# Kernel optimization log

Hardware: AMD Instinct MI355X
Metric: run time of the kernel (lower is better)

## Reference

```python
import jax, jax.numpy as jnp
import numpy as np

B, T, C = 2, 2048, 2048
N_HEAD, N_KV_HEAD = 16, 4
HEAD_DIM = C // N_HEAD          # 128
N_REP = N_HEAD // N_KV_HEAD     # 4
HALF = HEAD_DIM // 2            # 64


def setup_inputs() -> dict:
    key = jax.random.key(0)
    ks = jax.random.split(key, 6)
    x = jax.random.normal(ks[0], (B, T, C), dtype=jnp.float32)
    # real RoPE tables: theta_i = 10000^{-2i/d}, angles = t * theta_i
    inv_freq = 1.0 / (10000.0 ** (jnp.arange(0, HALF, dtype=jnp.float32) / HALF))
    angles = jnp.arange(T, dtype=jnp.float32)[:, None] * inv_freq[None, :]  # (T, HALF)
    freqs_cos = jnp.cos(angles)
    freqs_sin = jnp.sin(angles)
    s = 0.02
    wq = jax.random.normal(ks[1], (C, C), dtype=jnp.float32) * s
    wk = jax.random.normal(ks[2], (N_KV_HEAD * HEAD_DIM, C), dtype=jnp.float32) * s
    wv = jax.random.normal(ks[3], (N_KV_HEAD * HEAD_DIM, C), dtype=jnp.float32) * s
    wo = jax.random.normal(ks[4], (C, C), dtype=jnp.float32) * s
    return {"x": x, "freqs_cos": freqs_cos, "freqs_sin": freqs_sin,
            "wq": wq, "wk": wk, "wv": wv, "wo": wo}


def _apply_rope(t, cos, sin):
    # t: (B, T, H, D); rotate consecutive pairs (llama view_as_complex layout)
    te = t[..., 0::2]   # (B, T, H, D/2)
    to = t[..., 1::2]
    c = cos[None, :, None, :]
    s = sin[None, :, None, :]
    oe = te * c - to * s
    oo = te * s + to * c
    return jnp.stack([oe, oo], axis=-1).reshape(t.shape)


def reference(x, freqs_cos, freqs_sin, wq, wk, wv, wo):
    Bx, Tx, Cx = x.shape
    q = (x @ wq.T).reshape(Bx, Tx, N_HEAD, HEAD_DIM)
    k = (x @ wk.T).reshape(Bx, Tx, N_KV_HEAD, HEAD_DIM)
    v = (x @ wv.T).reshape(Bx, Tx, N_KV_HEAD, HEAD_DIM)
    q = _apply_rope(q, freqs_cos, freqs_sin)
    k = _apply_rope(k, freqs_cos, freqs_sin)
    # GQA: group query heads by kv head instead of repeat_interleave'ing KV
    qg = q.reshape(Bx, Tx, N_KV_HEAD, N_REP, HEAD_DIM)
    scale = 1.0 / jnp.sqrt(jnp.asarray(HEAD_DIM, dtype=q.dtype))
    # scores: (B, kv_head, rep, T, T)
    scores = jnp.einsum('btgrd,bsgd->bgrts', qg, k) * scale
    causal = jnp.tril(jnp.ones((Tx, Tx), dtype=bool))
    scores = jnp.where(causal[None, None, None], scores, jnp.asarray(-1e30, dtype=scores.dtype))
    probs = jax.nn.softmax(scores, axis=-1)
    y = jnp.einsum('bgrts,bsgd->btgrd', probs, v).reshape(Bx, Tx, Cx)
    return y @ wo.T
```

## Files before the change

### kernel.cpp

```cpp
#include <hip/hip_runtime.h>

#define T_SEQ 2048
#define NB    2
#define NHEAD 16
#define NKV   4
#define HD    128
#define CDIM  2048
#define QKV_W 3072
#define MROWS 4096

#define QSCALE 0.12752648137154393f

typedef unsigned int  uint;
typedef unsigned short ushort;

typedef __attribute__((ext_vector_type(8))) __bf16 bf16x8;
typedef __attribute__((ext_vector_type(4))) float  floatx4;

#if __has_builtin(__builtin_amdgcn_exp2f)
#define EXP2F(x) __builtin_amdgcn_exp2f(x)
#else
#define EXP2F(x) exp2f(x)
#endif

__device__ __forceinline__ uint bf16rne(float f) {
  uint u = __float_as_uint(f);
  u += 0x7fffu + ((u >> 16) & 1u);
  return u >> 16;
}
__device__ __forceinline__ float bflo(uint w) { return __uint_as_float(w << 16); }
__device__ __forceinline__ float bfhi(uint w) { return __uint_as_float(w & 0xffff0000u); }

__device__ __forceinline__ void block_bar() {
  __builtin_amdgcn_sched_barrier(0);
  __builtin_amdgcn_s_barrier();
  __builtin_amdgcn_sched_barrier(0);
}

__global__ void cast_all(const float* __restrict__ x,  const float* __restrict__ wq,
                         const float* __restrict__ wk, const float* __restrict__ wv,
                         const float* __restrict__ wo, uint* __restrict__ out) {
  int i = blockIdx.x * 256 + threadIdx.x;
  const float2* src; int off;
  if (i < 4194304)      { src = (const float2*)x;  off = 0; }
  else if (i < 6291456) { src = (const float2*)wq; off = 4194304; }
  else if (i < 6815744) { src = (const float2*)wk; off = 6291456; }
  else if (i < 7340032) { src = (const float2*)wv; off = 6815744; }
  else                  { src = (const float2*)wo; off = 7340032; }
  float2 v = src[i - off];
  out[i] = bf16rne(v.x) | (bf16rne(v.y) << 16);
}

__device__ __forceinline__ void store_elem(ushort* C, size_t idx, float v) { C[idx] = (ushort)bf16rne(v); }
__device__ __forceinline__ void store_elem(float*  C, size_t idx, float v) { C[idx] = v; }

template <typename OutT>
__global__ __launch_bounds__(256, 2) void gemm_bt(const ushort* __restrict__ A,
                                                  const ushort* __restrict__ Bt,
                                                  OutT* __restrict__ C,
                                                  int M, int N, int K,
                                                  int vcol0, ushort* __restrict__ vt) {
  __shared__ ushort smem[32768];
  const int tid  = threadIdx.x;
  const int wave = tid >> 6, lane = tid & 63;
  const int quad = lane >> 4, l16 = lane & 15;
  const int wm = wave >> 1, wn = wave & 1;
  const int mBase = blockIdx.y << 7;
  const int nBase = blockIdx.x << 7;
  const int NKT = K >> 6;

  floatx4 acc[4][4];
#pragma unroll
  for (int i = 0; i < 4; ++i)
#pragma unroll
    for (int j = 0; j < 4; ++j)
#pragma unroll
      for (int r = 0; r < 4; ++r) acc[i][j][r] = 0.f;

  const int srow = tid >> 3;
  const int sc8  = ((tid & 7) ^ (srow & 7)) << 3;
  const ushort* gA = A  + (size_t)(mBase + srow) * K + sc8;
  const ushort* gB = Bt + (size_t)(nBase + srow) * K + sc8;
  ushort* ldsA = smem + (wave << 9);
  ushort* ldsB = smem + 16384 + (wave << 9);

#define STAGE(k0, bsel)                                                               \
  do {                                                                                \
    _Pragma("unroll")                                                                 \
    for (int it_ = 0; it_ < 4; ++it_)                                                 \
      __builtin_amdgcn_global_load_lds(                                               \
          (const __attribute__((address_space(1))) void*)(gA + (size_t)it_ * 32 * K + (k0)), \
          (__attribute__((address_space(3))) void*)(ldsA + (bsel) + it_ * 2048), 16, 0, 0);  \
    _Pragma("unroll")                                                                 \
    for (int it_ = 0; it_ < 4; ++it_)                                                 \
      __builtin_amdgcn_global_load_lds(                                               \
          (const __attribute__((address_space(1))) void*)(gB + (size_t)it_ * 32 * K + (k0)), \
          (__attribute__((address_space(3))) void*)(ldsB + (bsel) + it_ * 2048), 16, 0, 0);  \
  } while (0)

  const int aro = ((wm << 6) + l16) * 64;
  const int bro = 16384 + ((wn << 6) + l16) * 64;
  const int sw0 = ((quad       ^ (l16 & 7)) << 3);
  const int sw1 = (((quad + 4) ^ (l16 & 7)) << 3);

  STAGE(0, 0);
  STAGE(64, 8192);
  asm volatile("s_waitcnt vmcnt(8)" ::: "memory");
  block_bar();

  for (int t = 0; t < NKT; ++t) {
    const int bsel = (t & 1) << 13;
#pragma unroll
    for (int kk = 0; kk < 2; ++kk) {
      const int sw = kk ? sw1 : sw0;
      bf16x8 bfrag[4];
#pragma unroll
      for (int j = 0; j < 4; ++j)
        bfrag[j] = *(const bf16x8*)&smem[bro + bsel + j * 1024 + sw];
#pragma unroll
      for (int i = 0; i < 4; ++i) {
        bf16x8 ai = *(const bf16x8*)&smem[aro + bsel + i * 1024 + sw];
#pragma unroll
        for (int j = 0; j < 4; ++j)
          acc[i][j] = __builtin_amdgcn_mfma_f32_16x16x32_bf16(ai, bfrag[j], acc[i][j], 0, 0, 0);
      }
    }
    asm volatile("s_waitcnt lgkmcnt(0)" ::: "memory");
    block_bar();
    if (t + 2 < NKT) {
      STAGE((t + 2) << 6, bsel);
      asm volatile("s_waitcnt vmcnt(8)" ::: "memory");
      block_bar();
    } else if (t + 1 < NKT) {
      asm volatile("s_waitcnt vmcnt(0)" ::: "memory");
      block_bar();
    }
  }
#undef STAGE

#pragma unroll
  for (int i = 0; i < 4; ++i) {
    const int rowb = mBase + (wm << 6) + (i << 4) + (quad << 2);
#pragma unroll
    for (int j = 0; j < 4; ++j) {
      const int colb = nBase + (wn << 6) + (j << 4);
      const int col  = colb + l16;
      if (colb < vcol0) {
#pragma unroll
        for (int r = 0; r < 4; ++r)
          store_elem(C, (size_t)(rowb + r) * N + col, acc[i][j][r]);
      } else {
        const int vcol = col - vcol0;
        const int bb = rowb >> 11;
        const int t  = rowb & 2047;
        uint2 pw;
        pw.x = bf16rne(acc[i][j][0]) | (bf16rne(acc[i][j][1]) << 16);
        pw.y = bf16rne(acc[i][j][2]) | (bf16rne(acc[i][j][3]) << 16);
        *(uint2*)(vt + (((size_t)(bb << 9) + vcol) << 11) + t) = pw;
      }
    }
  }
}

__global__ void rope_k(ushort* __restrict__ qkv, const float* __restrict__ fc,
                       const float* __restrict__ fs) {
  int idx  = blockIdx.x * 256 + threadIdx.x;
  int d2   = idx & 63;
  int rest = idx >> 6;
  int hh   = rest & 3;
  int bt   = rest >> 2;
  int t    = bt & (T_SEQ - 1);
  float c = fc[(t << 6) + d2];
  float s = fs[(t << 6) + d2];
  uint* p = (uint*)(qkv + (size_t)bt * QKV_W + 2048 + (hh << 7) + (d2 << 1));
  uint w = *p;
  float e = bflo(w), o = bfhi(w);
  *p = bf16rne(e * c - o * s) | (bf16rne(e * s + o * c) << 16);
}

__global__ __launch_bounds__(512, 2) void attn_mfma(const ushort* __restrict__ qkv,
                                                    const ushort* __restrict__ vtg,
                                                    ushort* __restrict__ y,
                                                    const float* __restrict__ fc,
                                                    const float* __restrict__ fs) {
  __shared__ ushort smem[51456];
  ushort* sP = smem + 32768;
  float*  sOf = (float*)smem;
  ushort* sO  = smem + 33792;
  float*  sLf = (float*)(smem + 51200);

  const int tid  = threadIdx.x;
  const int wave = tid >> 6, lane = tid & 63;
  const int quad = lane >> 4, l16 = lane & 15;
  const int w_s = wave & 1;
  const int w_t = wave >> 1;
  const int h = blockIdx.y, b = blockIdx.z, kh = h >> 2;
  const size_t bT = (size_t)b * T_SEQ;

  union { uint4 u; bf16x8 v; } ones_u;
  ones_u.u = make_uint4(0x3F803F80u, 0x3F803F80u, 0x3F803F80u, 0x3F803F80u);
  const bf16x8 onesf = ones_u.v;

  const int kr  = tid >> 4;
  const int kc8 = tid & 15;
  const ushort* gK = qkv + (bT + kr) * QKV_W + 2048 + kh * HD + ((kc8 ^ (kr & 7)) << 3);
  const int vd  = tid >> 3;
  const int vsc = tid & 7;
  const ushort* gV = vtg + (((size_t)(b << 9) + (kh << 7) + vd) << 11) + ((vsc ^ (vd & 7)) << 3);

#define STAGE_ATTN(cn, bo_)                                                            \
  do {                                                                                 \
    _Pragma("unroll")                                                                  \
    for (int it_ = 0; it_ < 2; ++it_)                                                  \
      __builtin_amdgcn_global_load_lds(                                                \
          (const __attribute__((address_space(1))) void*)(gK + ((size_t)(cn) * 64 + it_ * 32) * QKV_W), \
          (__attribute__((address_space(3))) void*)(smem + (bo_) + (wave << 9) + it_ * 4096), 16, 0, 0); \
    _Pragma("unroll")                                                                  \
    for (int it_ = 0; it_ < 2; ++it_)                                                  \
      __builtin_amdgcn_global_load_lds(                                                \
          (const __attribute__((address_space(1))) void*)(gV + ((size_t)it_ << 17) + (cn) * 64), \
          (__attribute__((address_space(3))) void*)(smem + 16384 + (bo_) + (wave << 9) + it_ * 4096), 16, 0, 0); \
  } while (0)

  for (int half = 0; half < 2; ++half) {
    const int xt = half ? (15 - (int)blockIdx.x) : (int)blockIdx.x;
    const int t0 = xt << 7;
    const int sblk = w_s << 5, tblk = w_t << 5;

    bf16x8 qf[2][4];
#pragma unroll
    for (int tt = 0; tt < 2; ++tt) {
      const int trow = t0 + tblk + tt * 16 + l16;
      const float* fcr = fc + (trow << 6);
      const float* fsr = fs + (trow << 6);
#pragma unroll
      for (int kk = 0; kk < 4; ++kk) {
        union { uint4 u; bf16x8 v; } qa;
        qa.u = *(const uint4*)(qkv + (bT + trow) * QKV_W + h * HD + kk * 32 + quad * 8);
        const int d2b = kk * 16 + quad * 4;
        uint* wp = (uint*)&qa.u;
#pragma unroll
        for (int m = 0; m < 4; ++m) {
          float c = fcr[d2b + m], s = fsr[d2b + m];
          float e = bflo(wp[m]), o = bfhi(wp[m]);
          float oe = (e * c - o * s) * QSCALE;
          float oo = (e * s + o * c) * QSCALE;
          wp[m] = bf16rne(oe) | (bf16rne(oo) << 16);
        }
        qf[tt][kk] = qa.v;
      }
    }

    floatx4 oacc[2][8];
    floatx4 lacc[2];
#pragma unroll
    for (int tt = 0; tt < 2; ++tt) {
#pragma unroll
      for (int r = 0; r < 4; ++r) lacc[tt][r] = 0.f;
#pragma unroll
      for (int dt = 0; dt < 8; ++dt)
#pragma unroll
        for (int r = 0; r < 4; ++r) oacc[tt][dt][r] = 0.f;
    }

    const int nch = (t0 >> 6) + 2;

    STAGE_ATTN(0, 0);

    for (int ch = 0; ch < nch; ++ch) {
      __syncthreads();
      if (ch + 1 < nch) STAGE_ATTN(ch + 1, ((ch + 1) & 1) << 13);
      const int bo = (ch & 1) << 13;
      const int s0 = ch << 6;

      const bool fullmask = (s0 + sblk) > (t0 + tblk + 31);
      if (!fullmask) {
        floatx4 accS[2][2];
#pragma unroll
        for (int st = 0; st < 2; ++st)
#pragma unroll
          for (int tt = 0; tt < 2; ++tt)
#pragma unroll
            for (int r = 0; r < 4; ++r) accS[st][tt][r] = 0.f;

#pragma unroll
        for (int kk = 0; kk < 4; ++kk) {
          bf16x8 kf0 = *(const bf16x8*)(smem + bo + (sblk + l16) * 128 +
                                        ((((kk << 2) + quad) ^ (l16 & 7)) << 3));
          bf16x8 kf1 = *(const bf16x8*)(smem + bo + (sblk + 16 + l16) * 128 +
                                        ((((kk << 2) + quad) ^ (l16 & 7)) << 3));
#pragma unroll
          for (int tt = 0; tt < 2; ++tt)
            accS[0][tt] = __builtin_amdgcn_mfma_f32_16x16x32_bf16(kf0, qf[tt][kk], accS[0][tt], 0, 0, 0);
#pragma unroll
          for (int tt = 0; tt < 2; ++tt)
            accS[1][tt] = __builtin_amdgcn_mfma_f32_16x16x32_bf16(kf1, qf[tt][kk], accS[1][tt], 0, 0, 0);
        }

        const bool diag = (s0 + sblk + 31) > (t0 + tblk);
#pragma unroll
        for (int st = 0; st < 2; ++st)
#pragma unroll
          for (int tt = 0; tt < 2; ++tt) {
            float p[4];
            if (diag) {
              const int sg = s0 + sblk + st * 16 + quad * 4;
              const int tg = t0 + tblk + tt * 16 + l16;
#pragma unroll
              for (int r = 0; r < 4; ++r)
                p[r] = (sg + r <= tg) ? EXP2F(accS[st][tt][r]) : 0.f;
            } else {
#pragma unroll
              for (int r = 0; r < 4; ++r) p[r] = EXP2F(accS[st][tt][r]);
            }
            uint2 pw;
            pw.x = (__float_as_uint(p[0]) >> 16) | (__float_as_uint(p[1]) & 0xFFFF0000u);
            pw.y = (__float_as_uint(p[2]) >> 16) | (__float_as_uint(p[3]) & 0xFFFF0000u);
            *(uint2*)(sP + (tblk + tt * 16 + l16) * 72 + sblk + st * 16 + quad * 4) = pw;
          }

        bf16x8 pf[2];
#pragma unroll
        for (int tt = 0; tt < 2; ++tt) {
          pf[tt] = *(const bf16x8*)(sP + (tblk + tt * 16 + l16) * 72 + sblk + (quad << 3));
          lacc[tt] = __builtin_amdgcn_mfma_f32_16x16x32_bf16(pf[tt], onesf, lacc[tt], 0, 0, 0);
        }
#pragma unroll
        for (int dt = 0; dt < 8; ++dt) {
          bf16x8 vf = *(const bf16x8*)(smem + 16384 + bo + (dt * 16 + l16) * 64 +
                                       ((((w_s << 2) + quad) ^ (l16 & 7)) << 3));
#pragma unroll
          for (int tt = 0; tt < 2; ++tt)
            oacc[tt][dt] = __builtin_amdgcn_mfma_f32_16x16x32_bf16(pf[tt], vf, oacc[tt][dt], 0, 0, 0);
        }
      }
    }

    __syncthreads();
    if (w_s == 0) {
#pragma unroll
      for (int tt = 0; tt < 2; ++tt) {
#pragma unroll
        for (int dt = 0; dt < 8; ++dt)
#pragma unroll
          for (int r = 0; r < 4; ++r)
            sOf[(tblk + tt * 16 + quad * 4 + r) * 132 + dt * 16 + l16] = oacc[tt][dt][r];
        if (l16 == 0) {
#pragma unroll
          for (int r = 0; r < 4; ++r)
            sLf[tblk + tt * 16 + quad * 4 + r] = lacc[tt][r];
        }
      }
    }
    __syncthreads();
    if (w_s == 1) {
#pragma unroll
      for (int tt = 0; tt < 2; ++tt) {
        float linv[4];
#pragma unroll
        for (int r = 0; r < 4; ++r)
          linv[r] = 1.0f / (sLf[tblk + tt * 16 + quad * 4 + r] + lacc[tt][r]);
#pragma unroll
        for (int dt = 0; dt < 8; ++dt)
#pragma unroll
          for (int r = 0; r < 4; ++r) {
            float v = (sOf[(tblk + tt * 16 + quad * 4 + r) * 132 + dt * 16 + l16] +
                       oacc[tt][dt][r]) * linv[r];
            sO[(tblk + tt * 16 + quad * 4 + r) * 136 + dt * 16 + l16] = (ushort)bf16rne(v);
          }
      }
    }
    __syncthreads();
#pragma unroll
    for (int it = 0; it < 4; ++it) {
      int idx = it * 512 + tid;
      int rr = idx >> 4, c8 = idx & 15;
      *(uint4*)(y + (bT + t0 + rr) * CDIM + h * HD + c8 * 8) =
          *(const uint4*)(sO + rr * 136 + c8 * 8);
    }
  }
#undef STAGE_ATTN
}

extern "C" void kernel_launch(void* const* d_in, const int* in_sizes, int n_in,
                              void* d_out, int out_size, void* d_ws, size_t ws_size,
                              hipStream_t stream) {
  const float* x    = (const float*)d_in[0];
  const float* fcos = (const float*)d_in[1];
  const float* fsin = (const float*)d_in[2];
  const float* wq   = (const float*)d_in[3];
  const float* wk   = (const float*)d_in[4];
  const float* wv   = (const float*)d_in[5];
  const float* wo   = (const float*)d_in[6];
  float* out = (float*)d_out;

  ushort* ws    = (ushort*)d_ws;
  ushort* xb    = ws;
  ushort* yb    = ws;
  ushort* wqkvb = ws    + 8388608;
  ushort* wob   = wqkvb + 6291456;
  ushort* qkv   = wob   + 4194304;
  ushort* vtg   = qkv   + 12582912;

  cast_all<<<36864, 256, 0, stream>>>(x, wq, wk, wv, wo, (uint*)ws);

  gemm_bt<ushort><<<dim3(QKV_W / 128, MROWS / 128), 256, 0, stream>>>(
      xb, wqkvb, qkv, MROWS, QKV_W, CDIM, 2560, vtg);

  rope_k<<<4096, 256, 0, stream>>>(qkv, fcos, fsin);

  attn_mfma<<<dim3(8, NHEAD, NB), 512, 0, stream>>>(qkv, vtg, yb, fcos, fsin);

  gemm_bt<float><<<dim3(CDIM / 128, MROWS / 128), 256, 0, stream>>>(
      yb, wob, out, MROWS, CDIM, CDIM, 1 << 30, nullptr);
}
```

Measured before the change: 278.2 us.

## Split attention blocks to one query tile each and shrink LDS for higher occupancy

Each attention block previously handled two query tiles (a paired long and short one for load balance). Now the grid doubles to 16 tiles per head and each block handles a single tile, launched in reverse order so the heaviest tiles start first. The P staging buffer moves to a 64-wide XOR-swizzled layout and the output reduction is done one 16-row slice at a time. Together these cut shared memory enough to raise launch bounds to 4 blocks per CU, trading the explicit pairing balance for more parallelism and occupancy, with added register pressure risk.

After: 372.6 us. +33.9%, slower.

```diff
diff --git a/kernel.cpp b/kernel.cpp
--- a/kernel.cpp
+++ b/kernel.cpp
@@ -178,16 +178,16 @@
   *p = bf16rne(e * c - o * s) | (bf16rne(e * s + o * c) << 16);
 }
 
-__global__ __launch_bounds__(512, 2) void attn_mfma(const ushort* __restrict__ qkv,
+__global__ __launch_bounds__(512, 4) void attn_mfma(const ushort* __restrict__ qkv,
                                                     const ushort* __restrict__ vtg,
                                                     ushort* __restrict__ y,
                                                     const float* __restrict__ fc,
                                                     const float* __restrict__ fs) {
-  __shared__ ushort smem[51456];
-  ushort* sP = smem + 32768;
+  __shared__ ushort smem[40960];
+  ushort* sP  = smem + 32768;
   float*  sOf = (float*)smem;
-  ushort* sO  = smem + 33792;
-  float*  sLf = (float*)(smem + 51200);
+  ushort* sO  = smem + 16896;
+  float*  sLf = (float*)(smem + 25600);
 
   const int tid  = threadIdx.x;
   const int wave = tid >> 6, lane = tid & 63;
@@ -222,161 +222,157 @@
           (__attribute__((address_space(3))) void*)(smem + 16384 + (bo_) + (wave << 9) + it_ * 4096), 16, 0, 0); \
   } while (0)
 
-  for (int half = 0; half < 2; ++half) {
-    const int xt = half ? (15 - (int)blockIdx.x) : (int)blockIdx.x;
-    const int t0 = xt << 7;
-    const int sblk = w_s << 5, tblk = w_t << 5;
-
-    bf16x8 qf[2][4];
-#pragma unroll
-    for (int tt = 0; tt < 2; ++tt) {
-      const int trow = t0 + tblk + tt * 16 + l16;
-      const float* fcr = fc + (trow << 6);
-      const float* fsr = fs + (trow << 6);
+  const int xt = 15 - (int)blockIdx.x;
+  const int t0 = xt << 7;
+  const int sblk = w_s << 5, tblk = w_t << 5;
+
+  bf16x8 qf[2][4];
+#pragma unroll
+  for (int tt = 0; tt < 2; ++tt) {
+    const int trow = t0 + tblk + tt * 16 + l16;
+    const float* fcr = fc + (trow << 6);
+    const float* fsr = fs + (trow << 6);
+#pragma unroll
+    for (int kk = 0; kk < 4; ++kk) {
+      union { uint4 u; bf16x8 v; } qa;
+      qa.u = *(const uint4*)(qkv + (bT + trow) * QKV_W + h * HD + kk * 32 + quad * 8);
+      const int d2b = kk * 16 + quad * 4;
+      uint* wp = (uint*)&qa.u;
+#pragma unroll
+      for (int m = 0; m < 4; ++m) {
+        float c = fcr[d2b + m], s = fsr[d2b + m];
+        float e = bflo(wp[m]), o = bfhi(wp[m]);
+        float oe = (e * c - o * s) * QSCALE;
+        float oo = (e * s + o * c) * QSCALE;
+        wp[m] = bf16rne(oe) | (bf16rne(oo) << 16);
+      }
+      qf[tt][kk] = qa.v;
+    }
+  }
+
+  floatx4 oacc[2][8];
+  floatx4 lacc[2];
+#pragma unroll
+  for (int tt = 0; tt < 2; ++tt) {
+#pragma unroll
+    for (int r = 0; r < 4; ++r) lacc[tt][r] = 0.f;
+#pragma unroll
+    for (int dt = 0; dt < 8; ++dt)
+#pragma unroll
+      for (int r = 0; r < 4; ++r) oacc[tt][dt][r] = 0.f;
+  }
+
+  const int nch = (t0 >> 6) + 2;
+
+  STAGE_ATTN(0, 0);
+
+  for (int ch = 0; ch < nch; ++ch) {
+    __syncthreads();
+    if (ch + 1 < nch) STAGE_ATTN(ch + 1, ((ch + 1) & 1) << 13);
+    const int bo = (ch & 1) << 13;
+    const int s0 = ch << 6;
+
+    const bool fullmask = (s0 + sblk) > (t0 + tblk + 31);
+    if (!fullmask) {
+      floatx4 accS[2][2];
+#pragma unroll
+      for (int st = 0; st < 2; ++st)
+#pragma unroll
+        for (int tt = 0; tt < 2; ++tt)
+#pragma unroll
+          for (int r = 0; r < 4; ++r) accS[st][tt][r] = 0.f;
+
 #pragma unroll
       for (int kk = 0; kk < 4; ++kk) {
-        union { uint4 u; bf16x8 v; } qa;
-        qa.u = *(const uint4*)(qkv + (bT + trow) * QKV_W + h * HD + kk * 32 + quad * 8);
-        const int d2b = kk * 16 + quad * 4;
-        uint* wp = (uint*)&qa.u;
-#pragma unroll
-        for (int m = 0; m < 4; ++m) {
-          float c = fcr[d2b + m], s = fsr[d2b + m];
-          float e = bflo(wp[m]), o = bfhi(wp[m]);
-          float oe = (e * c - o * s) * QSCALE;
-          float oo = (e * s + o * c) * QSCALE;
-          wp[m] = bf16rne(oe) | (bf16rne(oo) << 16);
+        bf16x8 kf0 = *(const bf16x8*)(smem + bo + (sblk + l16) * 128 +
+                                      ((((kk << 2) + quad) ^ (l16 & 7)) << 3));
+        bf16x8 kf1 = *(const bf16x8*)(smem + bo + (sblk + 16 + l16) * 128 +
+                                      ((((kk << 2) + quad) ^ (l16 & 7)) << 3));
+#pragma unroll
+        for (int tt = 0; tt < 2; ++tt)
+          accS[0][tt] = __builtin_amdgcn_mfma_f32_16x16x32_bf16(kf0, qf[tt][kk], accS[0][tt], 0, 0, 0);
+#pragma unroll
+        for (int tt = 0; tt < 2; ++tt)
+          accS[1][tt] = __builtin_amdgcn_mfma_f32_16x16x32_bf16(kf1, qf[tt][kk], accS[1][tt], 0, 0, 0);
+      }
+
+      const bool diag = (s0 + sblk + 31) > (t0 + tblk);
+#pragma unroll
+      for (int st = 0; st < 2; ++st)
+#pragma unroll
+        for (int tt = 0; tt < 2; ++tt) {
+          float p[4];
+          if (diag) {
+            const int sg = s0 + sblk + st * 16 + quad * 4;
+            const int tg = t0 + tblk + tt * 16 + l16;
+#pragma unroll
+            for (int r = 0; r < 4; ++r)
+              p[r] = (sg + r <= tg) ? EXP2F(accS[st][tt][r]) : 0.f;
+          } else {
+#pragma unroll
+            for (int r = 0; r < 4; ++r) p[r] = EXP2F(accS[st][tt][r]);
+          }
+          uint2 pw;
+          pw.x = (__float_as_uint(p[0]) >> 16) | (__float_as_uint(p[1]) & 0xFFFF0000u);
+          pw.y = (__float_as_uint(p[2]) >> 16) | (__float_as_uint(p[3]) & 0xFFFF0000u);
+          const int c4s = (((w_s << 3) + (st << 2) + quad) ^ ((l16 & 7) << 1)) << 2;
+          *(uint2*)(sP + ((tblk + tt * 16 + l16) << 6) + c4s) = pw;
         }
-        qf[tt][kk] = qa.v;
-      }
-    }
-
-    floatx4 oacc[2][8];
-    floatx4 lacc[2];
-#pragma unroll
-    for (int tt = 0; tt < 2; ++tt) {
-#pragma unroll
-      for (int r = 0; r < 4; ++r) lacc[tt][r] = 0.f;
+
+      bf16x8 pf[2];
+#pragma unroll
+      for (int tt = 0; tt < 2; ++tt) {
+        const int c4r = (((w_s << 3) + (quad << 1)) ^ ((l16 & 7) << 1)) << 2;
+        pf[tt] = *(const bf16x8*)(sP + ((tblk + tt * 16 + l16) << 6) + c4r);
+        lacc[tt] = __builtin_amdgcn_mfma_f32_16x16x32_bf16(pf[tt], onesf, lacc[tt], 0, 0, 0);
+      }
+#pragma unroll
+      for (int dt = 0; dt < 8; ++dt) {
+        bf16x8 vf = *(const bf16x8*)(smem + 16384 + bo + (dt * 16 + l16) * 64 +
+                                     ((((w_s << 2) + quad) ^ (l16 & 7)) << 3));
+#pragma unroll
+        for (int tt = 0; tt < 2; ++tt)
+          oacc[tt][dt] = __builtin_amdgcn_mfma_f32_16x16x32_bf16(pf[tt], vf, oacc[tt][dt], 0, 0, 0);
+      }
+    }
+  }
+
+#pragma unroll
+  for (int tt = 0; tt < 2; ++tt) {
+    __syncthreads();
+    const int v = (w_t << 4) + (quad << 2);
+    if (w_s == 0) {
 #pragma unroll
       for (int dt = 0; dt < 8; ++dt)
 #pragma unroll
-        for (int r = 0; r < 4; ++r) oacc[tt][dt][r] = 0.f;
-    }
-
-    const int nch = (t0 >> 6) + 2;
-
-    STAGE_ATTN(0, 0);
-
-    for (int ch = 0; ch < nch; ++ch) {
-      __syncthreads();
-      if (ch + 1 < nch) STAGE_ATTN(ch + 1, ((ch + 1) & 1) << 13);
-      const int bo = (ch & 1) << 13;
-      const int s0 = ch << 6;
-
-      const bool fullmask = (s0 + sblk) > (t0 + tblk + 31);
-      if (!fullmask) {
-        floatx4 accS[2][2];
-#pragma unroll
-        for (int st = 0; st < 2; ++st)
-#pragma unroll
-          for (int tt = 0; tt < 2; ++tt)
-#pragma unroll
-            for (int r = 0; r < 4; ++r) accS[st][tt][r] = 0.f;
-
-#pragma unroll
-        for (int kk = 0; kk < 4; ++kk) {
-          bf16x8 kf0 = *(const bf16x8*)(smem + bo + (sblk + l16) * 128 +
-                                        ((((kk << 2) + quad) ^ (l16 & 7)) << 3));
-          bf16x8 kf1 = *(const bf16x8*)(smem + bo + (sblk + 16 + l16) * 128 +
-                                        ((((kk << 2) + quad) ^ (l16 & 7)) << 3));
-#pragma unroll
-          for (int tt = 0; tt < 2; ++tt)
-            accS[0][tt] = __builtin_amdgcn_mfma_f32_16x16x32_bf16(kf0, qf[tt][kk], accS[0][tt], 0, 0, 0);
-#pragma unroll
-          for (int tt = 0; tt < 2; ++tt)
-            accS[1][tt] = __builtin_amdgcn_mfma_f32_16x16x32_bf16(kf1, qf[tt][kk], accS[1][tt], 0, 0, 0);
-        }
-
-        const bool diag = (s0 + sblk + 31) > (t0 + tblk);
-#pragma unroll
-        for (int st = 0; st < 2; ++st)
-#pragma unroll
-          for (int tt = 0; tt < 2; ++tt) {
-            float p[4];
-            if (diag) {
-              const int sg = s0 + sblk + st * 16 + quad * 4;
-              const int tg = t0 + tblk + tt * 16 + l16;
-#pragma unroll
-              for (int r = 0; r < 4; ++r)
-                p[r] = (sg + r <= tg) ? EXP2F(accS[st][tt][r]) : 0.f;
-            } else {
-#pragma unroll
-              for (int r = 0; r < 4; ++r) p[r] = EXP2F(accS[st][tt][r]);
-            }
-            uint2 pw;
-            pw.x = (__float_as_uint(p[0]) >> 16) | (__float_as_uint(p[1]) & 0xFFFF0000u);
-            pw.y = (__float_as_uint(p[2]) >> 16) | (__float_as_uint(p[3]) & 0xFFFF0000u);
-            *(uint2*)(sP + (tblk + tt * 16 + l16) * 72 + sblk + st * 16 + quad * 4) = pw;
-          }
-
-        bf16x8 pf[2];
-#pragma unroll
-        for (int tt = 0; tt < 2; ++tt) {
-          pf[tt] = *(const bf16x8*)(sP + (tblk + tt * 16 + l16) * 72 + sblk + (quad << 3));
-          lacc[tt] = __builtin_amdgcn_mfma_f32_16x16x32_bf16(pf[tt], onesf, lacc[tt], 0, 0, 0);
-        }
-#pragma unroll
-        for (int dt = 0; dt < 8; ++dt) {
-          bf16x8 vf = *(const bf16x8*)(smem + 16384 + bo + (dt * 16 + l16) * 64 +
-                                       ((((w_s << 2) + quad) ^ (l16 & 7)) << 3));
-#pragma unroll
-          for (int tt = 0; tt < 2; ++tt)
-            oacc[tt][dt] = __builtin_amdgcn_mfma_f32_16x16x32_bf16(pf[tt], vf, oacc[tt][dt], 0, 0, 0);
-        }
-      }
-    }
-
-    __syncthreads();
-    if (w_s == 0) {
-#pragma unroll
-      for (int tt = 0; tt < 2; ++tt) {
-#pragma unroll
-        for (int dt = 0; dt < 8; ++dt)
-#pragma unroll
-          for (int r = 0; r < 4; ++r)
-            sOf[(tblk + tt * 16 + quad * 4 + r) * 132 + dt * 16 + l16] = oacc[tt][dt][r];
-        if (l16 == 0) {
-#pragma unroll
-          for (int r = 0; r < 4; ++r)
-            sLf[tblk + tt * 16 + quad * 4 + r] = lacc[tt][r];
-        }
+        for (int r = 0; r < 4; ++r)
+          sOf[(v + r) * 132 + dt * 16 + l16] = oacc[tt][dt][r];
+      if (l16 == 0) {
+#pragma unroll
+        for (int r = 0; r < 4; ++r) sLf[v + r] = lacc[tt][r];
       }
     }
     __syncthreads();
     if (w_s == 1) {
-#pragma unroll
-      for (int tt = 0; tt < 2; ++tt) {
-        float linv[4];
-#pragma unroll
-        for (int r = 0; r < 4; ++r)
-          linv[r] = 1.0f / (sLf[tblk + tt * 16 + quad * 4 + r] + lacc[tt][r]);
-#pragma unroll
-        for (int dt = 0; dt < 8; ++dt)
-#pragma unroll
-          for (int r = 0; r < 4; ++r) {
-            float v = (sOf[(tblk + tt * 16 + quad * 4 + r) * 132 + dt * 16 + l16] +
-                       oacc[tt][dt][r]) * linv[r];
-            sO[(tblk + tt * 16 + quad * 4 + r) * 136 + dt * 16 + l16] = (ushort)bf16rne(v);
-          }
-      }
+      float linv[4];
+#pragma unroll
+      for (int r = 0; r < 4; ++r) linv[r] = 1.0f / (sLf[v + r] + lacc[tt][r]);
+#pragma unroll
+      for (int dt = 0; dt < 8; ++dt)
+#pragma unroll
+        for (int r = 0; r < 4; ++r) {
+          float val = (sOf[(v + r) * 132 + dt * 16 + l16] + oacc[tt][dt][r]) * linv[r];
+          sO[(v + r) * 136 + dt * 16 + l16] = (ushort)bf16rne(val);
+        }
     }
     __syncthreads();
 #pragma unroll
-    for (int it = 0; it < 4; ++it) {
+    for (int it = 0; it < 2; ++it) {
       int idx = it * 512 + tid;
-      int rr = idx >> 4, c8 = idx & 15;
+      int vv = idx >> 4, c8 = idx & 15;
+      int rr = ((vv >> 4) << 5) + tt * 16 + (vv & 15);
       *(uint4*)(y + (bT + t0 + rr) * CDIM + h * HD + c8 * 8) =
-          *(const uint4*)(sO + rr * 136 + c8 * 8);
+          *(const uint4*)(sO + vv * 136 + c8 * 8);
     }
   }
 #undef STAGE_ATTN
@@ -409,7 +405,7 @@
 
   rope_k<<<4096, 256, 0, stream>>>(qkv, fcos, fsin);
 
-  attn_mfma<<<dim3(8, NHEAD, NB), 512, 0, stream>>>(qkv, vtg, yb, fcos, fsin);
+  attn_mfma<<<dim3(16, NHEAD, NB), 512, 0, stream>>>(qkv, vtg, yb, fcos, fsin);
 
   gemm_bt<float><<<dim3(CDIM / 128, MROWS / 128), 256, 0, stream>>>(
       yb, wob, out, MROWS, CDIM, CDIM, 1 << 30, nullptr);
```
